# Optimization experiments

Measured on AMD Instinct MI355X. Metric: run time of the kernel, lower is better.

## Reference

```python
import jax, jax.numpy as jnp
import numpy as np

LC = 3  # number of multigrid levels


def injection1d(v):
    # fine -> coarse: take every other point, L -> (L+1)//2
    return v[..., ::2]


def interp1d(v):
    # coarse -> fine linear interpolation, L -> 2L-1
    B, C, N = v.shape
    out = jnp.zeros((B, C, 2 * N - 1), dtype=v.dtype)
    out = out.at[..., ::2].set(v)
    out = out.at[..., 1::2].set(0.5 * (v[..., :-1] + v[..., 1:]))
    return out


def mlp(xc, w1, c1, w2, c2, w3, c3):
    # pointwise (Conv1d kernel_size=1) MLP: [1 -> 64 -> 64 -> 1] with tanh
    h = jnp.tanh(jnp.einsum('oc,bcn->bon', w1, xc) + c1[:, None])
    h = jnp.tanh(jnp.einsum('oc,bcn->bon', w2, h) + c2[:, None])
    return jnp.einsum('oc,bcn->bon', w3, h) + c3[:, None]


def kernel_approximation(x, W1, b1, W2, b2, W3, b3):
    for _ in range(LC):
        x = injection1d(x)
    n = x.shape[-1]
    a = None
    n_ = 0
    for j in range(LC):
        band = mlp(x, W1[j], b1[j], W2[j], b2[j], W3[j], b3[j])  # (B, 1, n)
        if j == 0:
            a = band
            n_ = (n - 1) // 4
        else:
            a = a.at[..., n_:n_ + n].set(band)
            n_ = n_ * 2
        a = interp1d(a)
    return a  # (B, 1, 2N-1)


def toeplitz_mvp(a, u):
    # a: (B, 1, 2N-1) kernel values k(d), u: (B, 1, N)
    # w_i = sum_j a[N-1 + i - j] u_j  via circular FFT convolution of length 2N-1
    n = u.shape[-1]
    L = 2 * n - 1
    A = jnp.fft.rfft(a, n=L)
    U = jnp.fft.rfft(u, n=L)
    w = jnp.fft.irfft(A * U, n=L)
    return w[..., n - 1:]  # (B, 1, N)


def setup_inputs() -> dict:
    key = jax.random.key(0)
    ks = jax.random.split(key, 10)
    B, N = 1024, 8193
    u = jax.random.normal(ks[0], (B, 1, N), dtype=jnp.float32)
    # displacement coordinates in [-1, 1], length 2N-1, same for each batch row
    grid = jnp.linspace(-1.0, 1.0, 2 * N - 1, dtype=jnp.float32)
    x = jnp.broadcast_to(grid[None, None, :], (B, 1, 2 * N - 1)).astype(jnp.float32)
    # per-level MLP params, stacked over LC levels
    W1 = jax.random.normal(ks[1], (LC, 64, 1), dtype=jnp.float32) * 1.0
    b1 = jax.random.normal(ks[2], (LC, 64), dtype=jnp.float32) * 0.1
    W2 = jax.random.normal(ks[3], (LC, 64, 64), dtype=jnp.float32) * (1.0 / np.sqrt(64))
    b2 = jax.random.normal(ks[4], (LC, 64), dtype=jnp.float32) * 0.1
    W3 = jax.random.normal(ks[5], (LC, 1, 64), dtype=jnp.float32) * (1.0 / np.sqrt(64))
    b3 = jax.random.normal(ks[6], (LC, 1), dtype=jnp.float32) * 0.1
    return {"u": u, "x": x, "W1": W1, "b1": b1, "W2": W2, "b2": b2, "W3": W3, "b3": b3}


def reference(u, x, W1, b1, W2, b2, W3, b3):
    a = kernel_approximation(x, W1, b1, W2, b2, W3, b3)
    w = toeplitz_mvp(a, u)
    return w
```

## Files before the change

### kernel.cpp

```cpp
#include <hip/hip_runtime.h>

typedef unsigned short u16;
typedef unsigned int   u32;
typedef float  f32x4  __attribute__((ext_vector_type(4)));
typedef __bf16 bf16x8 __attribute__((ext_vector_type(8)));
typedef u16    u16x8  __attribute__((ext_vector_type(8)));

#define NB     1024
#define NN     8193
#define K2R    8256
#define NT     129
#define ABF_LEN 16704
#define NFRAG  1032

#define OFF_BANDS 0u
#define OFF_ABF   74496u
#define OFF_BFRAG 108032u
#define OFF_UREV  1175040u

__device__ __forceinline__ u16 f2bf(float f) {
  u32 u = __builtin_bit_cast(u32, f);
  return (u16)((u + 0x7FFFu + ((u >> 16) & 1u)) >> 16);
}
__device__ __forceinline__ float bf2f(u16 h) {
  u32 u = ((u32)h) << 16;
  return __builtin_bit_cast(float, u);
}

__global__ void k_bands(const float* __restrict__ x,
                        const float* __restrict__ W1, const float* __restrict__ b1,
                        const float* __restrict__ W2, const float* __restrict__ b2,
                        const float* __restrict__ W3, const float* __restrict__ b3,
                        float* __restrict__ bands) {
  const int j = blockIdx.y;
  __shared__ float w2s[4096];
  __shared__ float w1s[64], b1s[64], b2s[64], w3s[64];
  for (int i = threadIdx.x; i < 4096; i += 256) w2s[i] = W2[j * 4096 + i];
  if (threadIdx.x < 64) {
    w1s[threadIdx.x] = W1[j * 64 + threadIdx.x];
    b1s[threadIdx.x] = b1[j * 64 + threadIdx.x];
    b2s[threadIdx.x] = b2[j * 64 + threadIdx.x];
    w3s[threadIdx.x] = W3[j * 64 + threadIdx.x];
  }
  __syncthreads();
  const int k = blockIdx.x * 256 + threadIdx.x;
  if (k >= 2049) return;
  const float xc = x[8 * k];
  float h1[64];
  #pragma unroll
  for (int o = 0; o < 64; ++o) h1[o] = tanhf(w1s[o] * xc + b1s[o]);
  float outv = b3[j];
  for (int o = 0; o < 64; ++o) {
    float acc = b2s[o];
    #pragma unroll
    for (int c = 0; c < 64; ++c) acc += w2s[o * 64 + c] * h1[c];
    outv += w3s[o] * tanhf(acc);
  }
  bands[j * 2049 + k] = outv;
}

__global__ void k_interp(const float* __restrict__ bands, u16* __restrict__ abf) {
  __shared__ float s1[4097];
  __shared__ float s2[8193];
  const int tid = threadIdx.x;
  const float* bd0 = bands;
  const float* bd1 = bands + 2049;
  const float* bd2 = bands + 2 * 2049;
  for (int i = tid; i < 4097; i += 1024) {
    float v = (i & 1) ? 0.5f * (bd0[i >> 1] + bd0[(i >> 1) + 1]) : bd0[i >> 1];
    if (i >= 512 && i < 2561) v = bd1[i - 512];
    s1[i] = v;
  }
  __syncthreads();
  for (int i = tid; i < 8193; i += 1024) {
    float v = (i & 1) ? 0.5f * (s1[i >> 1] + s1[(i >> 1) + 1]) : s1[i >> 1];
    if (i >= 1024 && i < 3073) v = bd2[i - 1024];
    s2[i] = v;
  }
  __syncthreads();
  for (int i = tid; i < ABF_LEN; i += 1024) {
    float v = 0.f;
    if (i <= 16384)
      v = (i & 1) ? 0.5f * (s2[i >> 1] + s2[(i >> 1) + 1]) : s2[i >> 1];
    abf[i] = f2bf(v);
  }
}

__global__ void k_urev(const float* __restrict__ u, u16* __restrict__ urev) {
  const int b = blockIdx.y;
  const int c = blockIdx.x * 256 + threadIdx.x;
  if (c >= K2R / 8) return;
  const int j0 = c * 8;
  const float* ub = u + (size_t)b * NN;
  u16x8 v;
  #pragma unroll
  for (int r = 0; r < 8; ++r) {
    const int jr = j0 + r;
    const float f = (jr <= 8192) ? ub[8192 - jr] : 0.f;
    v[r] = f2bf(f);
  }
  *(u16x8*)&urev[(size_t)b * K2R + j0] = v;
}

__global__ void k_bfrag(const u16* __restrict__ abf, u16* __restrict__ bfr) {
  const int g = blockIdx.x * 256 + threadIdx.x;
  if (g >= NFRAG * 64) return;
  const int t = g >> 6, l = g & 63;
  const int s = 16 * t + (l & 15) + ((l >> 4) << 3);
  u16x8 v;
  #pragma unroll
  for (int r = 0; r < 8; ++r) v[r] = abf[s + r];
  *(u16x8*)&bfr[(size_t)g * 8] = v;
}

__global__ void k_lastcol(const u16* __restrict__ urev, const u16* __restrict__ abf,
                          float* __restrict__ out) {
  const int b = blockIdx.x;
  const int tid = threadIdx.x;
  float s = 0.f;
  #pragma unroll
  for (int it = 0; it < 5; ++it) {
    const int c = tid + 256 * it;
    if (c < K2R / 8) {
      u16x8 uv = *(const u16x8*)&urev[(size_t)b * K2R + c * 8];
      u16x8 av = *(const u16x8*)&abf[8192 + c * 8];
      #pragma unroll
      for (int r = 0; r < 8; ++r) s += bf2f(uv[r]) * bf2f(av[r]);
    }
  }
  #pragma unroll
  for (int off = 32; off >= 1; off >>= 1) s += __shfl_xor(s, off, 64);
  __shared__ float red[4];
  if ((tid & 63) == 0) red[tid >> 6] = s;
  __syncthreads();
  if (tid == 0) out[(size_t)b * NN + 8192] = red[0] + red[1] + red[2] + red[3];
}

__device__ __forceinline__ void gload16(const void* g, void* l) {
  __builtin_amdgcn_global_load_lds((__attribute__((address_space(1))) void*)(void*)g,
                                   (__attribute__((address_space(3))) void*)l, 16, 0, 0);
}

__global__ __launch_bounds__(256, 2) void k_gemm(const u16* __restrict__ urev,
                                                 const u16* __restrict__ bfrag,
                                                 float* __restrict__ out) {
  __shared__ u16 Ab[2][8192];
  __shared__ u16 Bb[2][6144];
  const int tid  = threadIdx.x;
  const int lane = tid & 63;
  const int wid  = tid >> 6;
  const int wr   = wid >> 1;
  const int wc   = wid & 1;

  const int by = blockIdx.x & 7;
  const int bx = blockIdx.x >> 3;
  const int b0 = by * 128;
  const int i0 = bx * 128;
  const int F0 = bx * 8;

  const u16* aSrc[4];
  #pragma unroll
  for (int r = 0; r < 4; ++r) {
    const int ch = tid + (r << 8);
    aSrc[r] = urev + (size_t)(b0 + (ch >> 3)) * K2R + (((ch & 7) ^ ((ch >> 3) & 7)) << 3);
  }
  const u16* bBase = bfrag + ((size_t)F0 << 9);

  f32x4 acc[4][4] = {};

  auto stage = [&](int buf, int t) {
    const int j0 = t << 6;
    #pragma unroll
    for (int r = 0; r < 4; ++r)
      gload16(aSrc[r] + j0, &Ab[buf][(tid + (r << 8)) << 3]);
    const u16* bs = bBase + ((size_t)t << 11);
    #pragma unroll
    for (int r = 0; r < 3; ++r) {
      const int ch = tid + (r << 8);
      gload16(bs + (ch << 3), &Bb[buf][ch << 3]);
    }
  };

  auto compute = [&](int buf) {
    bf16x8 af[8], bfv[8];
    #pragma unroll
    for (int kk = 0; kk < 2; ++kk)
      #pragma unroll
      for (int m = 0; m < 4; ++m) {
        const int row  = (wr << 6) + (m << 4) + (lane & 15);
        const int slot = ((lane >> 4) + (kk << 2)) ^ (row & 7);
        af[(kk << 2) + m] = *reinterpret_cast<const bf16x8*>(&Ab[buf][(row << 6) + (slot << 3)]);
      }
    #pragma unroll
    for (int kk = 0; kk < 2; ++kk)
      #pragma unroll
      for (int n = 0; n < 4; ++n) {
        const int w = (wc << 2) + n + (kk << 1);
        bfv[(kk << 2) + n] = *reinterpret_cast<const bf16x8*>(&Bb[buf][(w << 9) + (lane << 3)]);
      }
    #pragma unroll
    for (int kk = 0; kk < 2; ++kk)
      #pragma unroll
      for (int m = 0; m < 4; ++m)
        #pragma unroll
        for (int n = 0; n < 4; ++n)
          acc[m][n] = __builtin_amdgcn_mfma_f32_16x16x32_bf16(
              af[(kk << 2) + m], bfv[(kk << 2) + n], acc[m][n], 0, 0, 0);
  };

  stage(0, 0);
  asm volatile("s_waitcnt vmcnt(0)" ::: "memory");
  __syncthreads();
  int cur = 0;
  #pragma unroll 1
  for (int t = 0; t < NT - 1; ++t) {
    stage(cur ^ 1, t + 1);
    compute(cur);
    asm volatile("s_waitcnt vmcnt(0)" ::: "memory");
    __syncthreads();
    cur ^= 1;
  }
  compute(cur);

  #pragma unroll
  for (int n = 0; n < 4; ++n) {
    const int col = i0 + (wc << 6) + (n << 4) + (lane & 15);
    #pragma unroll
    for (int m = 0; m < 4; ++m) {
      const int rowb = b0 + (wr << 6) + (m << 4) + ((lane >> 4) << 2);
      float* o = out + (size_t)rowb * NN + col;
      #pragma unroll
      for (int r = 0; r < 4; ++r) o[(size_t)r * NN] = acc[m][n][r];
    }
  }
}

extern "C" void kernel_launch(void* const* d_in, const int* in_sizes, int n_in,
                              void* d_out, int out_size, void* d_ws, size_t ws_size,
                              hipStream_t stream) {
  (void)in_sizes; (void)n_in; (void)out_size; (void)ws_size;
  const float* u  = (const float*)d_in[0];
  const float* x  = (const float*)d_in[1];
  const float* W1 = (const float*)d_in[2];
  const float* b1 = (const float*)d_in[3];
  const float* W2 = (const float*)d_in[4];
  const float* b2 = (const float*)d_in[5];
  const float* W3 = (const float*)d_in[6];
  const float* b3 = (const float*)d_in[7];
  float* out = (float*)d_out;
  char*  ws  = (char*)d_ws;

  float* bands = (float*)(ws + OFF_BANDS);
  u16*   abf   = (u16*)(ws + OFF_ABF);
  u16*   bfr   = (u16*)(ws + OFF_BFRAG);
  u16*   urev  = (u16*)(ws + OFF_UREV);

  k_bands<<<dim3(9, 3), 256, 0, stream>>>(x, W1, b1, W2, b2, W3, b3, bands);
  k_interp<<<1, 1024, 0, stream>>>(bands, abf);
  k_urev<<<dim3(5, 1024), 256, 0, stream>>>(u, urev);
  k_bfrag<<<258, 256, 0, stream>>>(abf, bfr);
  k_lastcol<<<1024, 256, 0, stream>>>(urev, abf, out);
  k_gemm<<<512, 256, 0, stream>>>(urev, bfr, out);
}
```

Before: 225.3 us.

## Restructure GEMM main loop into phased ring-buffered B with split A staging

Replaces the double-buffered B tile with a 32-fragment ring buffer in LDS, exploiting that consecutive Toeplitz k-tiles share overlapping B fragments so only 4 new fragments are loaded per step instead of 6. Splits each k-step into two half-phases that interleave A global-to-LDS loads with LDS reads and MFMA bursts, using raw barriers, sched_barrier and setprio to control overlap. This aims to cut global/LDS traffic for B and hide load latency better, at the cost of more complex synchronization and a risk of ring-slot races if the wait counts are off.

```diff
diff --git a/kernel.cpp b/kernel.cpp
--- a/kernel.cpp
+++ b/kernel.cpp
@@ -145,7 +145,7 @@
                                                  const u16* __restrict__ bfrag,
                                                  float* __restrict__ out) {
   __shared__ u16 Ab[2][8192];
-  __shared__ u16 Bb[2][6144];
+  __shared__ u16 Bring[16384];
   const int tid  = threadIdx.x;
   const int lane = tid & 63;
   const int wid  = tid >> 6;
@@ -167,60 +167,99 @@
   const u16* bBase = bfrag + ((size_t)F0 << 9);
 
   f32x4 acc[4][4] = {};
-
-  auto stage = [&](int buf, int t) {
+  bf16x8 af[4], bv[4];
+
+  auto stageAhalf = [&](int buf, int t, int h) {
     const int j0 = t << 6;
     #pragma unroll
-    for (int r = 0; r < 4; ++r)
+    for (int r = 2 * h; r < 2 * h + 2; ++r)
       gload16(aSrc[r] + j0, &Ab[buf][(tid + (r << 8)) << 3]);
-    const u16* bs = bBase + ((size_t)t << 11);
-    #pragma unroll
-    for (int r = 0; r < 3; ++r) {
+  };
+  auto stageB = [&](int t) {
+    #pragma unroll
+    for (int r = 0; r < 2; ++r) {
       const int ch = tid + (r << 8);
-      gload16(bs + (ch << 3), &Bb[buf][ch << 3]);
-    }
-  };
-
-  auto compute = [&](int buf) {
-    bf16x8 af[8], bfv[8];
-    #pragma unroll
-    for (int kk = 0; kk < 2; ++kk)
+      const int fl = (t << 2) + 16 + (ch >> 6);
+      gload16(bBase + (((size_t)fl << 9) + ((ch & 63) << 3)),
+              &Bring[((fl & 31) << 9) + ((ch & 63) << 3)]);
+    }
+  };
+  auto dsreadA = [&](int buf, int kk) {
+    #pragma unroll
+    for (int m = 0; m < 4; ++m) {
+      const int row  = (wr << 6) + (m << 4) + (lane & 15);
+      const int slot = ((lane >> 4) + (kk << 2)) ^ (row & 7);
+      af[m] = *reinterpret_cast<const bf16x8*>(&Ab[buf][(row << 6) + (slot << 3)]);
+    }
+  };
+  auto dsreadB = [&](int t, int kk) {
+    #pragma unroll
+    for (int n = 0; n < 4; ++n) {
+      const int slot = ((t << 2) + (wc << 2) + n + (kk << 1)) & 31;
+      bv[n] = *reinterpret_cast<const bf16x8*>(&Bring[(slot << 9) + (lane << 3)]);
+    }
+  };
+  auto mfma16 = [&]() {
+    #pragma unroll
+    for (int m = 0; m < 4; ++m)
       #pragma unroll
-      for (int m = 0; m < 4; ++m) {
-        const int row  = (wr << 6) + (m << 4) + (lane & 15);
-        const int slot = ((lane >> 4) + (kk << 2)) ^ (row & 7);
-        af[(kk << 2) + m] = *reinterpret_cast<const bf16x8*>(&Ab[buf][(row << 6) + (slot << 3)]);
-      }
-    #pragma unroll
-    for (int kk = 0; kk < 2; ++kk)
-      #pragma unroll
-      for (int n = 0; n < 4; ++n) {
-        const int w = (wc << 2) + n + (kk << 1);
-        bfv[(kk << 2) + n] = *reinterpret_cast<const bf16x8*>(&Bb[buf][(w << 9) + (lane << 3)]);
-      }
-    #pragma unroll
-    for (int kk = 0; kk < 2; ++kk)
-      #pragma unroll
-      for (int m = 0; m < 4; ++m)
-        #pragma unroll
-        for (int n = 0; n < 4; ++n)
-          acc[m][n] = __builtin_amdgcn_mfma_f32_16x16x32_bf16(
-              af[(kk << 2) + m], bfv[(kk << 2) + n], acc[m][n], 0, 0, 0);
-  };
-
-  stage(0, 0);
+      for (int n = 0; n < 4; ++n)
+        acc[m][n] = __builtin_amdgcn_mfma_f32_16x16x32_bf16(af[m], bv[n], acc[m][n], 0, 0, 0);
+  };
+
+#define PH_TAIL()                                                \
+  __builtin_amdgcn_s_barrier();                                  \
+  asm volatile("s_waitcnt lgkmcnt(0)" ::: "memory");             \
+  __builtin_amdgcn_sched_barrier(0);                             \
+  __builtin_amdgcn_s_setprio(1);                                 \
+  mfma16();                                                      \
+  __builtin_amdgcn_s_setprio(0);
+
+  #pragma unroll
+  for (int r = 0; r < 4; ++r) {
+    const int ch = tid + (r << 8);
+    const int fl = ch >> 6;
+    gload16(bBase + (((size_t)fl << 9) + ((ch & 63) << 3)),
+            &Bring[(fl << 9) + ((ch & 63) << 3)]);
+  }
+  stageAhalf(0, 0, 0);
+  stageAhalf(0, 0, 1);
   asm volatile("s_waitcnt vmcnt(0)" ::: "memory");
-  __syncthreads();
-  int cur = 0;
+  __builtin_amdgcn_s_barrier();
+
   #pragma unroll 1
-  for (int t = 0; t < NT - 1; ++t) {
-    stage(cur ^ 1, t + 1);
-    compute(cur);
+  for (int t = 0; t < NT - 1; t += 2) {
+    dsreadA(0, 0); dsreadB(t, 0);
+    stageAhalf(1, t + 1, 0);
+    PH_TAIL();
+    __builtin_amdgcn_s_barrier();
+    dsreadA(0, 1); dsreadB(t, 1);
+    stageAhalf(1, t + 1, 1);
+    stageB(t);
+    PH_TAIL();
+    asm volatile("s_waitcnt vmcnt(2)" ::: "memory");
+    __builtin_amdgcn_s_barrier();
+
+    dsreadA(1, 0); dsreadB(t + 1, 0);
+    stageAhalf(0, t + 2, 0);
+    PH_TAIL();
+    __builtin_amdgcn_s_barrier();
+    dsreadA(1, 1); dsreadB(t + 1, 1);
+    stageAhalf(0, t + 2, 1);
+    PH_TAIL();
     asm volatile("s_waitcnt vmcnt(0)" ::: "memory");
-    __syncthreads();
-    cur ^= 1;
-  }
-  compute(cur);
+    __builtin_amdgcn_s_barrier();
+  }
+
+  dsreadA(0, 0); dsreadB(NT - 1, 0);
+  asm volatile("s_waitcnt lgkmcnt(0)" ::: "memory");
+  __builtin_amdgcn_sched_barrier(0);
+  mfma16();
+  dsreadA(0, 1); dsreadB(NT - 1, 1);
+  asm volatile("s_waitcnt lgkmcnt(0)" ::: "memory");
+  __builtin_amdgcn_sched_barrier(0);
+  mfma16();
+#undef PH_TAIL
 
   #pragma unroll
   for (int n = 0; n < 4; ++n) {
```

Measured after the change: 197.0 us. 12.6% less time.

## Rework Toeplitz GEMM to 32x32 MFMA with register-loaded B and phased pipeline

Applied to the files above, without the earlier changes.

The GEMM kernel moves from 16x16x32 to 32x32x16 bf16 MFMA tiles and now loads the Toeplitz B fragments straight from global memory into registers, double-banked, instead of staging them in LDS. The loop is split into explicit phases that interleave LDS reads, global prefetches, barriers and priority-raised MFMA bursts to overlap memory with compute. The B fragment layout and count are changed to match the 32-wide MFMA operand format. The MLP band kernel also splits its dot-product accumulation into four chains to raise ILP. In exchange the kernel carries more register pressure, and its correctness now depends on hand-placed waitcnt values.

```diff
diff --git a/kernel.cpp b/kernel.cpp
--- a/kernel.cpp
+++ b/kernel.cpp
@@ -2,7 +2,7 @@
 
 typedef unsigned short u16;
 typedef unsigned int   u32;
-typedef float  f32x4  __attribute__((ext_vector_type(4)));
+typedef float  f32x16 __attribute__((ext_vector_type(16)));
 typedef __bf16 bf16x8 __attribute__((ext_vector_type(8)));
 typedef u16    u16x8  __attribute__((ext_vector_type(8)));
 
@@ -11,7 +11,7 @@
 #define K2R    8256
 #define NT     129
 #define ABF_LEN 16704
-#define NFRAG  1032
+#define NFRAG  1040
 
 #define OFF_BANDS 0u
 #define OFF_ABF   74496u
@@ -51,10 +51,15 @@
   for (int o = 0; o < 64; ++o) h1[o] = tanhf(w1s[o] * xc + b1s[o]);
   float outv = b3[j];
   for (int o = 0; o < 64; ++o) {
-    float acc = b2s[o];
-    #pragma unroll
-    for (int c = 0; c < 64; ++c) acc += w2s[o * 64 + c] * h1[c];
-    outv += w3s[o] * tanhf(acc);
+    float a0 = 0.f, a1 = 0.f, a2 = 0.f, a3 = 0.f;
+    #pragma unroll
+    for (int c = 0; c < 64; c += 4) {
+      a0 += w2s[o * 64 + c] * h1[c];
+      a1 += w2s[o * 64 + c + 1] * h1[c + 1];
+      a2 += w2s[o * 64 + c + 2] * h1[c + 2];
+      a3 += w2s[o * 64 + c + 3] * h1[c + 3];
+    }
+    outv += w3s[o] * tanhf(b2s[o] + ((a0 + a1) + (a2 + a3)));
   }
   bands[j * 2049 + k] = outv;
 }
@@ -106,7 +111,7 @@
   const int g = blockIdx.x * 256 + threadIdx.x;
   if (g >= NFRAG * 64) return;
   const int t = g >> 6, l = g & 63;
-  const int s = 16 * t + (l & 15) + ((l >> 4) << 3);
+  const int s = 16 * t + (l & 31) + ((l >> 5) << 3);
   u16x8 v;
   #pragma unroll
   for (int r = 0; r < 8; ++r) v[r] = abf[s + r];
@@ -145,7 +150,6 @@
                                                  const u16* __restrict__ bfrag,
                                                  float* __restrict__ out) {
   __shared__ u16 Ab[2][8192];
-  __shared__ u16 Bb[2][6144];
   const int tid  = threadIdx.x;
   const int lane = tid & 63;
   const int wid  = tid >> 6;
@@ -164,75 +168,103 @@
     const int ch = tid + (r << 8);
     aSrc[r] = urev + (size_t)(b0 + (ch >> 3)) * K2R + (((ch & 7) ^ ((ch >> 3) & 7)) << 3);
   }
-  const u16* bBase = bfrag + ((size_t)F0 << 9);
-
-  f32x4 acc[4][4] = {};
-
-  auto stage = [&](int buf, int t) {
+  const u16* bW = bfrag + (((size_t)(F0 + (wc << 2))) << 9) + (lane << 3);
+
+  f32x16 acc[2][2] = {};
+  bf16x8 af[4];
+  bf16x8 bX[6], bY[6];
+
+  auto stageA = [&](int buf, int t) {
     const int j0 = t << 6;
     #pragma unroll
     for (int r = 0; r < 4; ++r)
       gload16(aSrc[r] + j0, &Ab[buf][(tid + (r << 8)) << 3]);
-    const u16* bs = bBase + ((size_t)t << 11);
-    #pragma unroll
-    for (int r = 0; r < 3; ++r) {
-      const int ch = tid + (r << 8);
-      gload16(bs + (ch << 3), &Bb[buf][ch << 3]);
+  };
+  auto loadB = [&](bf16x8* bk, int t) {
+    const u16* p = bW + ((size_t)t << 11);
+    #pragma unroll
+    for (int j = 0; j < 6; ++j)
+      bk[j] = *reinterpret_cast<const bf16x8*>(p + (j << 9));
+  };
+  auto dsA = [&](int buf, int p) {
+    #pragma unroll
+    for (int ktl = 0; ktl < 2; ++ktl)
+      #pragma unroll
+      for (int m = 0; m < 2; ++m) {
+        const int row  = (wr << 6) + (m << 5) + (lane & 31);
+        const int kt   = (p << 1) + ktl;
+        const int slot = ((lane >> 5) + (kt << 1)) ^ (row & 7);
+        af[(ktl << 1) + m] = *reinterpret_cast<const bf16x8*>(&Ab[buf][(row << 6) + (slot << 3)]);
+      }
+  };
+  auto mm8 = [&](const bf16x8* bk, int p) {
+    #pragma unroll
+    for (int ktl = 0; ktl < 2; ++ktl)
+      #pragma unroll
+      for (int m = 0; m < 2; ++m)
+        #pragma unroll
+        for (int n = 0; n < 2; ++n)
+          acc[m][n] = __builtin_amdgcn_mfma_f32_32x32x16_bf16(
+              af[(ktl << 1) + m], bk[(n << 1) + (p << 1) + ktl], acc[m][n], 0, 0, 0);
+  };
+
+#define PHASE(dbuf, pp, bank, ISSUE, TAIL)                        \
+  {                                                               \
+    dsA(dbuf, pp);                                                \
+    __builtin_amdgcn_sched_barrier(0);                            \
+    ISSUE;                                                        \
+    __builtin_amdgcn_sched_barrier(0);                            \
+    __builtin_amdgcn_s_barrier();                                 \
+    asm volatile("s_waitcnt lgkmcnt(0)" ::: "memory");            \
+    __builtin_amdgcn_sched_barrier(0);                            \
+    __builtin_amdgcn_s_setprio(1);                                \
+    mm8(bank, pp);                                                \
+    __builtin_amdgcn_s_setprio(0);                                \
+    __builtin_amdgcn_sched_barrier(0);                            \
+    TAIL;                                                         \
+    __builtin_amdgcn_s_barrier();                                 \
+  }
+
+  stageA(0, 0);
+  __builtin_amdgcn_sched_barrier(0);
+  loadB(bX, 0);
+  __builtin_amdgcn_sched_barrier(0);
+  asm volatile("s_waitcnt vmcnt(6)" ::: "memory");
+  __builtin_amdgcn_s_barrier();
+
+  #pragma unroll 1
+  for (int t = 0; t < NT - 1; t += 2) {
+    PHASE(0, 0, bX, stageA(1, t + 1), );
+    PHASE(0, 1, bX, loadB(bY, t + 1),
+          asm volatile("s_waitcnt vmcnt(6)" ::: "memory"));
+    PHASE(1, 0, bY, stageA(0, t + 2), );
+    PHASE(1, 1, bY, loadB(bX, t + 2),
+          asm volatile("s_waitcnt vmcnt(6)" ::: "memory"));
+  }
+#undef PHASE
+
+  dsA(0, 0);
+  asm volatile("s_waitcnt lgkmcnt(0)" ::: "memory");
+  __builtin_amdgcn_sched_barrier(0);
+  mm8(bX, 0);
+  dsA(0, 1);
+  asm volatile("s_waitcnt lgkmcnt(0)" ::: "memory");
+  __builtin_amdgcn_sched_barrier(0);
+  mm8(bX, 1);
+
+  const int cb = i0 + (wc << 6) + (lane & 31);
+  const int rb = b0 + (wr << 6) + ((lane >> 5) << 2);
+  #pragma unroll
+  for (int m = 0; m < 2; ++m)
+    #pragma unroll
+    for (int n = 0; n < 2; ++n) {
+      #pragma unroll
+      for (int r = 0; r < 16; ++r) {
+        const int row = rb + (m << 5) + (r & 3) + ((r >> 2) << 3);
+        const int col = cb + (n << 5);
+        out[(size_t)row * NN + col] = acc[m][n][r];
+      }
     }
-  };
-
-  auto compute = [&](int buf) {
-    bf16x8 af[8], bfv[8];
-    #pragma unroll
-    for (int kk = 0; kk < 2; ++kk)
-      #pragma unroll
-      for (int m = 0; m < 4; ++m) {
-        const int row  = (wr << 6) + (m << 4) + (lane & 15);
-        const int slot = ((lane >> 4) + (kk << 2)) ^ (row & 7);
-        af[(kk << 2) + m] = *reinterpret_cast<const bf16x8*>(&Ab[buf][(row << 6) + (slot << 3)]);
-      }
-    #pragma unroll
-    for (int kk = 0; kk < 2; ++kk)
-      #pragma unroll
-      for (int n = 0; n < 4; ++n) {
-        const int w = (wc << 2) + n + (kk << 1);
-        bfv[(kk << 2) + n] = *reinterpret_cast<const bf16x8*>(&Bb[buf][(w << 9) + (lane << 3)]);
-      }
-    #pragma unroll
-    for (int kk = 0; kk < 2; ++kk)
-      #pragma unroll
-      for (int m = 0; m < 4; ++m)
-        #pragma unroll
-        for (int n = 0; n < 4; ++n)
-          acc[m][n] = __builtin_amdgcn_mfma_f32_16x16x32_bf16(
-              af[(kk << 2) + m], bfv[(kk << 2) + n], acc[m][n], 0, 0, 0);
-  };
-
-  stage(0, 0);
-  asm volatile("s_waitcnt vmcnt(0)" ::: "memory");
-  __syncthreads();
-  int cur = 0;
-  #pragma unroll 1
-  for (int t = 0; t < NT - 1; ++t) {
-    stage(cur ^ 1, t + 1);
-    compute(cur);
-    asm volatile("s_waitcnt vmcnt(0)" ::: "memory");
-    __syncthreads();
-    cur ^= 1;
-  }
-  compute(cur);
-
-  #pragma unroll
-  for (int n = 0; n < 4; ++n) {
-    const int col = i0 + (wc << 6) + (n << 4) + (lane & 15);
-    #pragma unroll
-    for (int m = 0; m < 4; ++m) {
-      const int rowb = b0 + (wr << 6) + (m << 4) + ((lane >> 4) << 2);
-      float* o = out + (size_t)rowb * NN + col;
-      #pragma unroll
-      for (int r = 0; r < 4; ++r) o[(size_t)r * NN] = acc[m][n][r];
-    }
-  }
 }
 
 extern "C" void kernel_launch(void* const* d_in, const int* in_sizes, int n_in,
@@ -258,7 +290,7 @@
   k_bands<<<dim3(9, 3), 256, 0, stream>>>(x, W1, b1, W2, b2, W3, b3, bands);
   k_interp<<<1, 1024, 0, stream>>>(bands, abf);
   k_urev<<<dim3(5, 1024), 256, 0, stream>>>(u, urev);
-  k_bfrag<<<258, 256, 0, stream>>>(abf, bfr);
+  k_bfrag<<<260, 256, 0, stream>>>(abf, bfr);
   k_lastcol<<<1024, 256, 0, stream>>>(urev, abf, out);
   k_gemm<<<512, 256, 0, stream>>>(urev, bfr, out);
 }
```

Result: faster. 209.3 us (-7.1%).

## Load GEMM operands directly to registers, vectorize urev, split MLP accumulators

Applied to the files above, without the earlier changes.

The GEMM drops its LDS double buffer and barriers: each wave loads its A rows and B fragments straight from global memory into register double buffers (aX/aY, bX/bY), software-pipelined two steps per iteration. The aim is to remove LDS traffic and __syncthreads stalls, relying on L2/L1 to serve the duplicated loads across waves. This raises register pressure and global load volume. k_urev now uses float4 loads for the reversal, and the k_bands inner dot product uses four independent accumulators to shorten the dependency chain.

```diff
diff --git a/kernel.cpp b/kernel.cpp
--- a/kernel.cpp
+++ b/kernel.cpp
@@ -51,10 +51,15 @@
   for (int o = 0; o < 64; ++o) h1[o] = tanhf(w1s[o] * xc + b1s[o]);
   float outv = b3[j];
   for (int o = 0; o < 64; ++o) {
-    float acc = b2s[o];
-    #pragma unroll
-    for (int c = 0; c < 64; ++c) acc += w2s[o * 64 + c] * h1[c];
-    outv += w3s[o] * tanhf(acc);
+    float a0 = 0.f, a1 = 0.f, a2 = 0.f, a3 = 0.f;
+    #pragma unroll
+    for (int c = 0; c < 64; c += 4) {
+      a0 += w2s[o * 64 + c] * h1[c];
+      a1 += w2s[o * 64 + c + 1] * h1[c + 1];
+      a2 += w2s[o * 64 + c + 2] * h1[c + 2];
+      a3 += w2s[o * 64 + c + 3] * h1[c + 3];
+    }
+    outv += w3s[o] * tanhf(b2s[o] + ((a0 + a1) + (a2 + a3)));
   }
   bands[j * 2049 + k] = outv;
 }
@@ -93,11 +98,21 @@
   const int j0 = c * 8;
   const float* ub = u + (size_t)b * NN;
   u16x8 v;
-  #pragma unroll
-  for (int r = 0; r < 8; ++r) {
-    const int jr = j0 + r;
-    const float f = (jr <= 8192) ? ub[8192 - jr] : 0.f;
-    v[r] = f2bf(f);
+  if (j0 < 8192) {
+    const int e = 8192 - j0;
+    const float4 q0 = *(const float4*)&ub[e - 8];
+    const float4 q1 = *(const float4*)&ub[e - 4];
+    const float  s  = ub[e];
+    v[0] = f2bf(s);
+    v[1] = f2bf(q1.w); v[2] = f2bf(q1.z); v[3] = f2bf(q1.y); v[4] = f2bf(q1.x);
+    v[5] = f2bf(q0.w); v[6] = f2bf(q0.z); v[7] = f2bf(q0.y);
+  } else if (j0 == 8192) {
+    v[0] = f2bf(ub[0]);
+    #pragma unroll
+    for (int r = 1; r < 8; ++r) v[r] = 0;
+  } else {
+    #pragma unroll
+    for (int r = 0; r < 8; ++r) v[r] = 0;
   }
   *(u16x8*)&urev[(size_t)b * K2R + j0] = v;
 }
@@ -136,16 +151,9 @@
   if (tid == 0) out[(size_t)b * NN + 8192] = red[0] + red[1] + red[2] + red[3];
 }
 
-__device__ __forceinline__ void gload16(const void* g, void* l) {
-  __builtin_amdgcn_global_load_lds((__attribute__((address_space(1))) void*)(void*)g,
-                                   (__attribute__((address_space(3))) void*)l, 16, 0, 0);
-}
-
 __global__ __launch_bounds__(256, 2) void k_gemm(const u16* __restrict__ urev,
                                                  const u16* __restrict__ bfrag,
                                                  float* __restrict__ out) {
-  __shared__ u16 Ab[2][8192];
-  __shared__ u16 Bb[2][6144];
   const int tid  = threadIdx.x;
   const int lane = tid & 63;
   const int wid  = tid >> 6;
@@ -158,46 +166,28 @@
   const int i0 = bx * 128;
   const int F0 = bx * 8;
 
-  const u16* aSrc[4];
-  #pragma unroll
-  for (int r = 0; r < 4; ++r) {
-    const int ch = tid + (r << 8);
-    aSrc[r] = urev + (size_t)(b0 + (ch >> 3)) * K2R + (((ch & 7) ^ ((ch >> 3) & 7)) << 3);
-  }
-  const u16* bBase = bfrag + ((size_t)F0 << 9);
+  const u16* aRow = urev + (size_t)(b0 + (wr << 6) + (lane & 15)) * K2R + ((lane >> 4) << 3);
+  const u16* bW = bfrag + (((size_t)(F0 + (wc << 2))) << 9) + (lane << 3);
 
   f32x4 acc[4][4] = {};
-
-  auto stage = [&](int buf, int t) {
-    const int j0 = t << 6;
-    #pragma unroll
-    for (int r = 0; r < 4; ++r)
-      gload16(aSrc[r] + j0, &Ab[buf][(tid + (r << 8)) << 3]);
-    const u16* bs = bBase + ((size_t)t << 11);
-    #pragma unroll
-    for (int r = 0; r < 3; ++r) {
-      const int ch = tid + (r << 8);
-      gload16(bs + (ch << 3), &Bb[buf][ch << 3]);
-    }
+  bf16x8 aX[8], aY[8], bX[6], bY[6];
+
+  auto loadA = [&](bf16x8* ar, int t) {
+    const u16* p = aRow + (t << 6);
+    #pragma unroll
+    for (int kk = 0; kk < 2; ++kk)
+      #pragma unroll
+      for (int m = 0; m < 4; ++m)
+        ar[(kk << 2) + m] = *reinterpret_cast<const bf16x8*>(
+            p + (size_t)m * (16 * K2R) + (kk << 5));
   };
-
-  auto compute = [&](int buf) {
-    bf16x8 af[8], bfv[8];
-    #pragma unroll
-    for (int kk = 0; kk < 2; ++kk)
-      #pragma unroll
-      for (int m = 0; m < 4; ++m) {
-        const int row  = (wr << 6) + (m << 4) + (lane & 15);
-        const int slot = ((lane >> 4) + (kk << 2)) ^ (row & 7);
-        af[(kk << 2) + m] = *reinterpret_cast<const bf16x8*>(&Ab[buf][(row << 6) + (slot << 3)]);
-      }
-    #pragma unroll
-    for (int kk = 0; kk < 2; ++kk)
-      #pragma unroll
-      for (int n = 0; n < 4; ++n) {
-        const int w = (wc << 2) + n + (kk << 1);
-        bfv[(kk << 2) + n] = *reinterpret_cast<const bf16x8*>(&Bb[buf][(w << 9) + (lane << 3)]);
-      }
+  auto loadB = [&](bf16x8* br, int t) {
+    const u16* p = bW + ((size_t)t << 11);
+    #pragma unroll
+    for (int j = 0; j < 6; ++j)
+      br[j] = *reinterpret_cast<const bf16x8*>(p + (j << 9));
+  };
+  auto mm = [&](const bf16x8* ar, const bf16x8* br) {
     #pragma unroll
     for (int kk = 0; kk < 2; ++kk)
       #pragma unroll
@@ -205,22 +195,20 @@
         #pragma unroll
         for (int n = 0; n < 4; ++n)
           acc[m][n] = __builtin_amdgcn_mfma_f32_16x16x32_bf16(
-              af[(kk << 2) + m], bfv[(kk << 2) + n], acc[m][n], 0, 0, 0);
+              ar[(kk << 2) + m], br[n + (kk << 1)], acc[m][n], 0, 0, 0);
   };
 
-  stage(0, 0);
-  asm volatile("s_waitcnt vmcnt(0)" ::: "memory");
-  __syncthreads();
-  int cur = 0;
+  loadA(aX, 0);
+  loadB(bX, 0);
+
   #pragma unroll 1
-  for (int t = 0; t < NT - 1; ++t) {
-    stage(cur ^ 1, t + 1);
-    compute(cur);
-    asm volatile("s_waitcnt vmcnt(0)" ::: "memory");
-    __syncthreads();
-    cur ^= 1;
-  }
-  compute(cur);
+  for (int t = 0; t < NT - 1; t += 2) {
+    loadA(aY, t + 1); loadB(bY, t + 1);
+    mm(aX, bX);
+    loadA(aX, t + 2); loadB(bX, t + 2);
+    mm(aY, bY);
+  }
+  mm(aX, bX);
 
   #pragma unroll
   for (int n = 0; n < 4; ++n) {
```

New measurement: 330.9 us. +46.9%, slower.
